# Optimization experiments

Measured on AMD Instinct MI355X. Metric: run time of the kernel, lower is better.

The kernel has to match this reference:

```python
import jax, jax.numpy as jnp
import numpy as np
import itertools

B, T, C, H = 2, 2048, 1024, 8
HD = C // H  # head_dim = 128


def _head_dirs():
    # 8 trigrams = vertices of cube {-1,+1}^3, L2-normalized (norm sqrt(3))
    signs = [-1.0, 1.0]
    tri = np.array(list(itertools.product(signs, repeat=3)), dtype=np.float32)
    tri = tri / np.linalg.norm(tri, axis=1, keepdims=True)
    return jnp.asarray(tri[:H])  # [H, 3]


def setup_inputs() -> dict:
    key = jax.random.key(0)
    ks = jax.random.split(key, 5)
    w = lambda k, sh: jax.random.normal(k, sh, dtype=jnp.float32) * 0.02
    return {
        "x": jax.random.normal(ks[0], (B, T, C), dtype=jnp.float32),
        "Wq": w(ks[1], (H * 3, C)),
        "Wk": w(ks[2], (H * 3, C)),
        "Wv": w(ks[3], (C, C)),
        "Wo": w(ks[4], (C, C)),
        "scale": jnp.asarray(1.0 / np.sqrt(3.0), dtype=jnp.float32),
    }


def reference(x, Wq, Wk, Wv, Wo, scale):
    Bb, Tt, Cc = x.shape
    dirs = _head_dirs()  # [H, 3] constant buffer
    # tiny 3-dim per-head Q/K projections
    q3 = (x @ Wq.T).reshape(Bb, Tt, H, 3).transpose(0, 2, 1, 3)  # [B,H,T,3]
    k3 = (x @ Wk.T).reshape(Bb, Tt, H, 3).transpose(0, 2, 1, 3)  # [B,H,T,3]
    v = (x @ Wv.T).reshape(Bb, Tt, H, HD).transpose(0, 2, 1, 3)  # [B,H,T,HD]
    # projections of q/k onto each head's trigram direction
    q_on_dir = jnp.einsum('bhtd,hd->bht', q3, dirs)  # [B,H,T]
    k_on_dir = jnp.einsum('bhtd,hd->bht', k3, dirs)  # [B,H,T]
    # scores = scaled 3-dim dot product + geometric outer-product bias
    scores = jnp.einsum('bhtd,bhsd->bhts', q3, k3) * scale \
        + q_on_dir[..., :, None] * k_on_dir[..., None, :]  # [B,H,T,T]
    causal = jnp.tril(jnp.ones((Tt, Tt), dtype=bool))
    scores = jnp.where(causal, scores, -jnp.inf)
    attn = jax.nn.softmax(scores, axis=-1)
    out = jnp.einsum('bhts,bhsd->bhtd', attn, v)  # [B,H,T,HD]
    out = out.transpose(0, 2, 1, 3).reshape(Bb, Tt, Cc)
    return out @ Wo.T
```

## Files before the change

### kernel.cpp

```cpp
#include <hip/hip_runtime.h>
#include <hip/hip_bf16.h>

#define B_  2
#define T_  2048
#define C_  1024
#define H_  8
#define HD_ 128
#define M_  (B_*T_)

typedef short  bf16x8 __attribute__((ext_vector_type(8)));
typedef float  f32x4  __attribute__((ext_vector_type(4)));
typedef unsigned short u16x8 __attribute__((ext_vector_type(8)));
typedef unsigned int   u32x4 __attribute__((ext_vector_type(4)));

typedef const __attribute__((address_space(1))) void* gas_ptr;
typedef __attribute__((address_space(3))) void*       las_ptr;

#define L2E_ 1.4426950408889634f

static __device__ __forceinline__ unsigned short f2bf(float f) {
    unsigned int u = __float_as_uint(f);
    u += 0x7fffu + ((u >> 16) & 1u);
    return (unsigned short)(u >> 16);
}
static __device__ __forceinline__ unsigned int rne_u32(float f) {
    unsigned int u = __float_as_uint(f);
    return u + 0x7fffu + ((u >> 16) & 1u);
}
static __device__ __forceinline__ float bf2f(unsigned short u) {
    return __uint_as_float(((unsigned int)u) << 16);
}
static __device__ __forceinline__ float exp2_fast(float x) {
#if __has_builtin(__builtin_amdgcn_exp2f)
    return __builtin_amdgcn_exp2f(x);
#else
    return exp2f(x);
#endif
}

__global__ __launch_bounds__(256) void k_convert_w(const float* __restrict__ Wv,
                                                   const float* __restrict__ Wo,
                                                   unsigned short* __restrict__ wvbf,
                                                   unsigned short* __restrict__ wobf) {
    int i = blockIdx.x * 256 + threadIdx.x;
    const float* src; unsigned short* dst; int off;
    if (i < 262144) { src = Wv; dst = wvbf; off = i; }
    else            { src = Wo; dst = wobf; off = i - 262144; }
    float4 v = reinterpret_cast<const float4*>(src)[off];
    ushort4 o;
    o.x = f2bf(v.x); o.y = f2bf(v.y); o.z = f2bf(v.z); o.w = f2bf(v.w);
    reinterpret_cast<ushort4*>(dst)[off] = o;
}

__global__ __launch_bounds__(256) void k_proj_qk(const float* __restrict__ x,
                                                 const float* __restrict__ Wq,
                                                 const float* __restrict__ Wk,
                                                 const float* __restrict__ scale_p,
                                                 float* __restrict__ qt,
                                                 float* __restrict__ kt,
                                                 unsigned short* __restrict__ xbf) {
    __shared__ __align__(16) float wl[48][260];
    __shared__ __align__(16) float xl[16][260];
    __shared__ float res[16][48];
    const int tid  = threadIdx.x;
    const int row0 = blockIdx.x << 4;
    const int r    = tid >> 4, sub = tid & 15;
    float a0 = 0.f, a1 = 0.f, a2 = 0.f;

    for (int ch = 0; ch < 4; ++ch) {
        const int k0 = ch * 256;
        #pragma unroll
        for (int i = 0; i < 12; ++i) {
            int fi = i * 256 + tid;
            int wr = fi >> 6, wc = (fi & 63) * 4;
            const float* src = (wr < 24) ? (Wq + (size_t)wr * C_) : (Wk + (size_t)(wr - 24) * C_);
            *reinterpret_cast<float4*>(&wl[wr][wc]) = *reinterpret_cast<const float4*>(src + k0 + wc);
        }
        #pragma unroll
        for (int i = 0; i < 4; ++i) {
            int fi = i * 256 + tid;
            int xr = fi >> 6, xc = (fi & 63) * 4;
            size_t goff = (size_t)(row0 + xr) * C_ + k0 + xc;
            float4 xv = *reinterpret_cast<const float4*>(x + goff);
            *reinterpret_cast<float4*>(&xl[xr][xc]) = xv;
            ushort4 o;
            o.x = f2bf(xv.x); o.y = f2bf(xv.y); o.z = f2bf(xv.z); o.w = f2bf(xv.w);
            *reinterpret_cast<ushort4*>(xbf + goff) = o;
        }
        __syncthreads();
        const int oc = sub * 3;
        #pragma unroll 4
        for (int k = 0; k < 256; k += 4) {
            float4 xv = *reinterpret_cast<const float4*>(&xl[r][k]);
            float4 w0 = *reinterpret_cast<const float4*>(&wl[oc + 0][k]);
            float4 w1 = *reinterpret_cast<const float4*>(&wl[oc + 1][k]);
            float4 w2 = *reinterpret_cast<const float4*>(&wl[oc + 2][k]);
            a0 += xv.x * w0.x + xv.y * w0.y + xv.z * w0.z + xv.w * w0.w;
            a1 += xv.x * w1.x + xv.y * w1.y + xv.z * w1.z + xv.w * w1.w;
            a2 += xv.x * w2.x + xv.y * w2.y + xv.z * w2.z + xv.w * w2.w;
        }
        __syncthreads();
    }
    res[r][sub * 3 + 0] = a0;
    res[r][sub * 3 + 1] = a1;
    res[r][sub * 3 + 2] = a2;
    __syncthreads();

    {
        const int rr = tid >> 4, s2 = tid & 15;
        const int isK = s2 >> 3, h = s2 & 7;
        const float r3 = 0.57735026918962576f;
        float d0 = (h & 4) ? r3 : -r3;
        float d1 = (h & 2) ? r3 : -r3;
        float d2 = (h & 1) ? r3 : -r3;
        const float* v3 = &res[rr][isK * 24 + h * 3];
        float a = v3[0], b = v3[1], c = v3[2];
        float ond = a * d0 + b * d1 + c * d2;
        float sc = scale_p[0];
        float4 ov = isK ? make_float4(a, b, c, ond)
                        : make_float4(a * sc * L2E_, b * sc * L2E_, c * sc * L2E_, ond * L2E_);
        float* dst = isK ? kt : qt;
        int grow = row0 + rr;
        int b_ = grow >> 11, t_idx = grow & (T_ - 1);
        reinterpret_cast<float4*>(dst)[(size_t)(b_ * H_ + h) * T_ + t_idx] = ov;
    }
}

template <int MODE>
__global__ __launch_bounds__(256) void k_gemm128x64(const unsigned short* __restrict__ A,
                                                    const unsigned short* __restrict__ Bw,
                                                    void* __restrict__ Cout,
                                                    int Mdim, int Ndim, int Kdim) {
    __shared__ __align__(16) unsigned short lds_a[8][128][8];
    __shared__ __align__(16) unsigned short lds_b[8][64][8];
    const int tid = threadIdx.x;
    const int nbn = Ndim >> 6;
    const int bm = (blockIdx.x / nbn) << 7;
    const int bn = (blockIdx.x % nbn) << 6;
    const int w = tid >> 6, l = tid & 63;
    const int wm = (w >> 1) << 6, wn = (w & 1) << 5;
    const int lh = l & 15, lq = l >> 4;

    f32x4 acc[4][2];
    #pragma unroll
    for (int i = 0; i < 4; ++i)
        #pragma unroll
        for (int j = 0; j < 2; ++j)
            acc[i][j] = (f32x4){0.f, 0.f, 0.f, 0.f};

    for (int k0 = 0; k0 < Kdim; k0 += 64) {
        #pragma unroll
        for (int p = 0; p < 4; ++p) {
            int flat = p * 256 + tid;
            int kq = flat >> 7, row = flat & 127;
            __builtin_amdgcn_global_load_lds((gas_ptr)(A + (size_t)(bm + row) * Kdim + k0 + kq * 8),
                (las_ptr)(&lds_a[0][0][0] + (size_t)flat * 8), 16, 0, 0);
        }
        #pragma unroll
        for (int p = 0; p < 2; ++p) {
            int flat = p * 256 + tid;
            int kq = flat >> 6, row = flat & 63;
            __builtin_amdgcn_global_load_lds((gas_ptr)(Bw + (size_t)(bn + row) * Kdim + k0 + kq * 8),
                (las_ptr)(&lds_b[0][0][0] + (size_t)flat * 8), 16, 0, 0);
        }
        __syncthreads();

        #pragma unroll
        for (int kk = 0; kk < 2; ++kk) {
            bf16x8 af[4], bfr[2];
            #pragma unroll
            for (int f = 0; f < 4; ++f)
                af[f] = *reinterpret_cast<const bf16x8*>(&lds_a[lq + 4 * kk][wm + f * 16 + lh][0]);
            #pragma unroll
            for (int f = 0; f < 2; ++f)
                bfr[f] = *reinterpret_cast<const bf16x8*>(&lds_b[lq + 4 * kk][wn + f * 16 + lh][0]);
            #pragma unroll
            for (int i = 0; i < 4; ++i)
                #pragma unroll
                for (int j = 0; j < 2; ++j)
                    acc[i][j] = __builtin_amdgcn_mfma_f32_16x16x32_bf16(af[i], bfr[j], acc[i][j], 0, 0, 0);
        }
        __syncthreads();
    }

    if constexpr (MODE == 0) {
        float* Cf = (float*)Cout;
        #pragma unroll
        for (int i = 0; i < 4; ++i) {
            int rbase = bm + wm + i * 16 + lq * 4;
            #pragma unroll
            for (int j = 0; j < 2; ++j) {
                int cidx = bn + wn + j * 16 + lh;
                #pragma unroll
                for (int r = 0; r < 4; ++r)
                    Cf[(size_t)(rbase + r) * Ndim + cidx] = acc[i][j][r];
            }
        }
    } else {
        __shared__ unsigned short ldsT[128][72];
        #pragma unroll
        for (int i = 0; i < 4; ++i)
            #pragma unroll
            for (int j = 0; j < 2; ++j)
                #pragma unroll
                for (int r = 0; r < 4; ++r)
                    ldsT[wm + i * 16 + lq * 4 + r][wn + j * 16 + lh] = f2bf(acc[i][j][r]);
        __syncthreads();
        unsigned short* vt_out = (unsigned short*)Cout;
        int c = tid & 63, part = tid >> 6;
        int b = bm >> 11, t0 = bm & (T_ - 1);
        unsigned short* dst = vt_out + ((size_t)b * C_ + bn + c) * T_ + t0 + part * 32;
        #pragma unroll
        for (int jj = 0; jj < 4; ++jj) {
            u16x8 v;
            #pragma unroll
            for (int k = 0; k < 8; ++k) v[k] = ldsT[part * 32 + jj * 8 + k][c];
            *reinterpret_cast<u16x8*>(dst + jj * 8) = v;
        }
    }
}

__global__ __launch_bounds__(256) void k_attn64(
        const float4* __restrict__ qt, const float4* __restrict__ kt,
        const unsigned short* __restrict__ vt,
        unsigned short* __restrict__ mpart,
        float2* __restrict__ mlbuf,
        int nsp, int lg2nsp) {
    __shared__ __align__(16) unsigned short lv[2][8192];
    __shared__ __align__(16) float4 lk[2][64];
    const int tid = threadIdx.x;
    const int w = tid >> 6, l = tid & 63;
    const int lh = l & 15, lg = l >> 4;
    const int bid = blockIdx.x;
    const int qb = 31 - (bid >> (4 + lg2nsp));
    const int sp = (bid >> 4) & (nsp - 1);
    const int bh = bid & 15;
    const int q0 = qb << 6;
    const int qrow = q0 + 4 * lh + w;
    const int nt = qb + 1;

    const float4* qtb = qt + (size_t)bh * T_;
    const float4* ktb = kt + (size_t)bh * T_;
    const unsigned short* vtb = vt + (size_t)bh * HD_ * T_;

    const unsigned short* vsrc[4];
    #pragma unroll
    for (int i = 0; i < 4; ++i) {
        int f = i * 256 + tid;
        vsrc[i] = vtb + (size_t)((((f >> 6) & 7) * 16) + (f & 15)) * T_
                      + ((f >> 9) << 5) + ((f >> 4) & 3) * 8;
    }

#define STAGE(ST, BUF) do {                                                    \
    int s0_ = (ST) << 6;                                                       \
    __builtin_amdgcn_global_load_lds((gas_ptr)(vsrc[0] + s0_),                 \
        (las_ptr)(&lv[BUF][0] + (size_t)(0 * 256 + tid) * 8), 16, 0, 0);       \
    __builtin_amdgcn_global_load_lds((gas_ptr)(vsrc[1] + s0_),                 \
        (las_ptr)(&lv[BUF][0] + (size_t)(1 * 256 + tid) * 8), 16, 0, 0);       \
    __builtin_amdgcn_global_load_lds((gas_ptr)(vsrc[2] + s0_),                 \
        (las_ptr)(&lv[BUF][0] + (size_t)(2 * 256 + tid) * 8), 16, 0, 0);       \
    __builtin_amdgcn_global_load_lds((gas_ptr)(vsrc[3] + s0_),                 \
        (las_ptr)(&lv[BUF][0] + (size_t)(3 * 256 + tid) * 8), 16, 0, 0);       \
    __builtin_amdgcn_global_load_lds((gas_ptr)(ktb + s0_ + l),                 \
        (las_ptr)(&lk[BUF][0]), 16, 0, 0);                                     \
} while (0)

    const float4 q4 = qtb[qrow];
    f32x4 acc[8];
    #pragma unroll
    for (int n = 0; n < 8; ++n) acc[n] = (f32x4){0.f, 0.f, 0.f, 0.f};
    float m = -1e30f, lsum = 0.f;

    if (sp < nt) STAGE(sp, 0);
    __syncthreads();

    int buf = 0;
    for (int st = sp; st < nt; st += nsp) {
        if (st + nsp < nt) STAGE(st + nsp, buf ^ 1);

        const int s0 = st << 6;
        const int c0 = s0 + lg * 8;
        const int c1 = s0 + 32 + lg * 8;

        float p[16];
        if (st != qb) {
            #pragma unroll
            for (int jj = 0; jj < 8; ++jj) {
                float4 k4 = lk[buf][lg * 8 + jj];
                p[jj] = fmaf(q4.x, k4.x, fmaf(q4.y, k4.y, fmaf(q4.z, k4.z, q4.w * k4.w)));
            }
            #pragma unroll
            for (int jj = 0; jj < 8; ++jj) {
                float4 k4 = lk[buf][32 + lg * 8 + jj];
                p[8 + jj] = fmaf(q4.x, k4.x, fmaf(q4.y, k4.y, fmaf(q4.z, k4.z, q4.w * k4.w)));
            }
        } else {
            #pragma unroll
            for (int jj = 0; jj < 8; ++jj) {
                float4 k4 = lk[buf][lg * 8 + jj];
                float sc = fmaf(q4.x, k4.x, fmaf(q4.y, k4.y, fmaf(q4.z, k4.z, q4.w * k4.w)));
                p[jj] = (c0 + jj > qrow) ? -1e30f : sc;
            }
            #pragma unroll
            for (int jj = 0; jj < 8; ++jj) {
                float4 k4 = lk[buf][32 + lg * 8 + jj];
                float sc = fmaf(q4.x, k4.x, fmaf(q4.y, k4.y, fmaf(q4.z, k4.z, q4.w * k4.w)));
                p[8 + jj] = (c1 + jj > qrow) ? -1e30f : sc;
            }
        }

        float ma = fmaxf(fmaxf(p[0], p[1]), p[2]);
        float mb = fmaxf(fmaxf(p[3], p[4]), p[5]);
        float mc = fmaxf(fmaxf(p[6], p[7]), p[8]);
        float md = fmaxf(fmaxf(p[9], p[10]), p[11]);
        float me = fmaxf(fmaxf(p[12], p[13]), p[14]);
        float mt = fmaxf(fmaxf(fmaxf(ma, mb), fmaxf(mc, md)), fmaxf(me, p[15]));
        mt = fmaxf(mt, __shfl_xor(mt, 16));
        mt = fmaxf(mt, __shfl_xor(mt, 32));
        if (__any(mt > m + 8.f)) {
            float mnew = fmaxf(m, mt);
            float corr = exp2_fast(m - mnew);
            m = mnew;
            lsum *= corr;
            float cc0 = __shfl(corr, 4 * lg + 0);
            float cc1 = __shfl(corr, 4 * lg + 1);
            float cc2 = __shfl(corr, 4 * lg + 2);
            float cc3 = __shfl(corr, 4 * lg + 3);
            #pragma unroll
            for (int n = 0; n < 8; ++n) {
                acc[n][0] *= cc0; acc[n][1] *= cc1; acc[n][2] *= cc2; acc[n][3] *= cc3;
            }
        }
        #pragma unroll
        for (int jj = 0; jj < 16; ++jj)
            p[jj] = exp2_fast(p[jj] - m);
        float sa = (p[0] + p[1] + p[2]) + (p[3] + p[4] + p[5]);
        float sb = (p[6] + p[7] + p[8]) + (p[9] + p[10] + p[11]);
        float ps = sa + sb + ((p[12] + p[13] + p[14]) + p[15]);
        ps += __shfl_xor(ps, 16);
        ps += __shfl_xor(ps, 32);
        lsum += ps;

        u32x4 w0, w1;
        #pragma unroll
        for (int i = 0; i < 4; ++i) {
            w0[i] = __builtin_amdgcn_perm(rne_u32(p[2 * i + 1]), rne_u32(p[2 * i]), 0x07060302u);
            w1[i] = __builtin_amdgcn_perm(rne_u32(p[8 + 2 * i + 1]), rne_u32(p[8 + 2 * i]), 0x07060302u);
        }
        bf16x8 pa0 = __builtin_bit_cast(bf16x8, w0);
        bf16x8 pa1 = __builtin_bit_cast(bf16x8, w1);

        #pragma unroll
        for (int n = 0; n < 8; ++n) {
            bf16x8 vf = *reinterpret_cast<const bf16x8*>(&lv[buf][(size_t)(n * 64 + lg * 16 + lh) * 8]);
            acc[n] = __builtin_amdgcn_mfma_f32_16x16x32_bf16(pa0, vf, acc[n], 0, 0, 0);
        }
        #pragma unroll
        for (int n = 0; n < 8; ++n) {
            bf16x8 vf = *reinterpret_cast<const bf16x8*>(&lv[buf][(size_t)(512 + n * 64 + lg * 16 + lh) * 8]);
            acc[n] = __builtin_amdgcn_mfma_f32_16x16x32_bf16(pa1, vf, acc[n], 0, 0, 0);
        }

        __syncthreads();
        buf ^= 1;
    }
#undef STAGE

    unsigned short* mp = mpart + (size_t)(sp * 16 + bh) * T_ * HD_;
    #pragma unroll
    for (int n = 0; n < 8; ++n) {
        #pragma unroll
        for (int r = 0; r < 4; ++r) {
            int row = q0 + 16 * lg + 4 * r + w;
            mp[(size_t)row * HD_ + n * 16 + lh] = f2bf(acc[n][r]);
        }
    }
    if (lg == 0)
        mlbuf[(size_t)(sp * 16 + bh) * T_ + qrow] = make_float2(m, lsum);
}

__global__ __launch_bounds__(256) void k_combine(const unsigned short* __restrict__ mpart,
                                                 const float2* __restrict__ mlbuf,
                                                 unsigned short* __restrict__ attnbf,
                                                 int nsp) {
    int idx = blockIdx.x * 256 + threadIdx.x;
    int bh = idx >> 16;
    int rem = idx & 65535;
    int t = rem >> 5, d0 = (rem & 31) * 4;
    float mg = -1e30f, den = 0.f;
    float ax = 0.f, ay = 0.f, az = 0.f, aw = 0.f;
    for (int s = 0; s < nsp; ++s) {
        float2 ml = mlbuf[(size_t)(s * 16 + bh) * T_ + t];
        ushort4 a = *reinterpret_cast<const ushort4*>(
            mpart + ((size_t)(s * 16 + bh) * T_ + t) * HD_ + d0);
        float mn = fmaxf(mg, ml.x);
        float cOld = exp2_fast(mg - mn);
        float cNew = exp2_fast(ml.x - mn);
        den = den * cOld + ml.y * cNew;
        ax = ax * cOld + bf2f(a.x) * cNew;
        ay = ay * cOld + bf2f(a.y) * cNew;
        az = az * cOld + bf2f(a.z) * cNew;
        aw = aw * cOld + bf2f(a.w) * cNew;
        mg = mn;
    }
    float inv = 1.f / den;
    int b = bh >> 3, h = bh & 7;
    ushort4 o;
    o.x = f2bf(ax * inv); o.y = f2bf(ay * inv);
    o.z = f2bf(az * inv); o.w = f2bf(aw * inv);
    *reinterpret_cast<ushort4*>(attnbf + ((size_t)(b * T_ + t) * C_ + h * HD_ + d0)) = o;
}

extern "C" void kernel_launch(void* const* d_in, const int* in_sizes, int n_in,
                              void* d_out, int out_size, void* d_ws, size_t ws_size,
                              hipStream_t stream) {
    const float* x     = (const float*)d_in[0];
    const float* Wq    = (const float*)d_in[1];
    const float* Wk    = (const float*)d_in[2];
    const float* Wv    = (const float*)d_in[3];
    const float* Wo    = (const float*)d_in[4];
    const float* scale = (const float*)d_in[5];
    float* out = (float*)d_out;

    const int nsp    = (ws_size >= 46137344) ? 4 : 2;
    const int lg2nsp = (nsp == 4) ? 2 : 1;

    char* ws = (char*)d_ws;
    size_t o = (size_t)nsp * 8388608;
    unsigned short* mpart  = (unsigned short*)(ws);
    unsigned short* xbf    = (unsigned short*)(ws);
    unsigned short* wvbf   = (unsigned short*)(ws + 8388608);
    float*          qt     = (float*)(ws + o);
    float*          kt     = (float*)(ws + o + 524288);
    unsigned short* vt     = (unsigned short*)(ws + o + 1048576);
    unsigned short* attnbf = (unsigned short*)(ws + o + 1048576);
    unsigned short* wobf   = (unsigned short*)(ws + o + 9437184);
    float2*         mlbuf  = (float2*)(ws + o + 11534336);

    k_convert_w<<<2048, 256, 0, stream>>>(Wv, Wo, wvbf, wobf);

    k_proj_qk<<<M_ / 16, 256, 0, stream>>>(x, Wq, Wk, scale, qt, kt, xbf);

    k_gemm128x64<2><<<(M_ / 128) * (C_ / 64), 256, 0, stream>>>(xbf, wvbf, (void*)vt, M_, C_, C_);

    k_attn64<<<32 * nsp * 16, 256, 0, stream>>>(
        reinterpret_cast<const float4*>(qt), reinterpret_cast<const float4*>(kt), vt,
        mpart, mlbuf, nsp, lg2nsp);

    k_combine<<<4096, 256, 0, stream>>>(mpart, mlbuf, attnbf, nsp);

    k_gemm128x64<0><<<(M_ / 128) * (C_ / 64), 256, 0, stream>>>(attnbf, wobf, (void*)out, M_, C_, C_);
}
```

Before: 133.8 us.

## Double-buffer LDS tiles in the 128x64 GEMM to overlap loads with MFMA

Adds a second LDS buffer for the A and B tiles of the bf16 GEMM kernel. The next K-slice is issued with global_load_lds while MFMAs run on the current buffer, with one barrier per iteration instead of two. The goal is to hide global memory latency in the projection GEMMs. In exchange, the kernel's LDS use roughly doubles, which can lower how many blocks fit per CU.

```diff
diff --git a/kernel.cpp b/kernel.cpp
--- a/kernel.cpp
+++ b/kernel.cpp
@@ -131,8 +131,8 @@
                                                     const unsigned short* __restrict__ Bw,
                                                     void* __restrict__ Cout,
                                                     int Mdim, int Ndim, int Kdim) {
-    __shared__ __align__(16) unsigned short lds_a[8][128][8];
-    __shared__ __align__(16) unsigned short lds_b[8][64][8];
+    __shared__ __align__(16) unsigned short lds_a[2][8][128][8];
+    __shared__ __align__(16) unsigned short lds_b[2][8][64][8];
     const int tid = threadIdx.x;
     const int nbn = Ndim >> 6;
     const int bm = (blockIdx.x / nbn) << 7;
@@ -141,6 +141,25 @@
     const int wm = (w >> 1) << 6, wn = (w & 1) << 5;
     const int lh = l & 15, lq = l >> 4;
 
+#define GSTAGE(K0, BUF) do {                                                          \
+    _Pragma("unroll")                                                                 \
+    for (int p_ = 0; p_ < 4; ++p_) {                                                  \
+        int flat_ = p_ * 256 + tid;                                                   \
+        int kq_ = flat_ >> 7, row_ = flat_ & 127;                                     \
+        __builtin_amdgcn_global_load_lds(                                             \
+            (gas_ptr)(A + (size_t)(bm + row_) * Kdim + (K0) + kq_ * 8),               \
+            (las_ptr)(&lds_a[BUF][0][0][0] + (size_t)flat_ * 8), 16, 0, 0);           \
+    }                                                                                 \
+    _Pragma("unroll")                                                                 \
+    for (int p_ = 0; p_ < 2; ++p_) {                                                  \
+        int flat_ = p_ * 256 + tid;                                                   \
+        int kq_ = flat_ >> 6, row_ = flat_ & 63;                                      \
+        __builtin_amdgcn_global_load_lds(                                             \
+            (gas_ptr)(Bw + (size_t)(bn + row_) * Kdim + (K0) + kq_ * 8),              \
+            (las_ptr)(&lds_b[BUF][0][0][0] + (size_t)flat_ * 8), 16, 0, 0);           \
+    }                                                                                 \
+} while (0)
+
     f32x4 acc[4][2];
     #pragma unroll
     for (int i = 0; i < 4; ++i)
@@ -148,32 +167,22 @@
         for (int j = 0; j < 2; ++j)
             acc[i][j] = (f32x4){0.f, 0.f, 0.f, 0.f};
 
+    GSTAGE(0, 0);
+    __syncthreads();
+
+    int buf = 0;
     for (int k0 = 0; k0 < Kdim; k0 += 64) {
-        #pragma unroll
-        for (int p = 0; p < 4; ++p) {
-            int flat = p * 256 + tid;
-            int kq = flat >> 7, row = flat & 127;
-            __builtin_amdgcn_global_load_lds((gas_ptr)(A + (size_t)(bm + row) * Kdim + k0 + kq * 8),
-                (las_ptr)(&lds_a[0][0][0] + (size_t)flat * 8), 16, 0, 0);
-        }
-        #pragma unroll
-        for (int p = 0; p < 2; ++p) {
-            int flat = p * 256 + tid;
-            int kq = flat >> 6, row = flat & 63;
-            __builtin_amdgcn_global_load_lds((gas_ptr)(Bw + (size_t)(bn + row) * Kdim + k0 + kq * 8),
-                (las_ptr)(&lds_b[0][0][0] + (size_t)flat * 8), 16, 0, 0);
-        }
-        __syncthreads();
+        if (k0 + 64 < Kdim) GSTAGE(k0 + 64, buf ^ 1);
 
         #pragma unroll
         for (int kk = 0; kk < 2; ++kk) {
             bf16x8 af[4], bfr[2];
             #pragma unroll
             for (int f = 0; f < 4; ++f)
-                af[f] = *reinterpret_cast<const bf16x8*>(&lds_a[lq + 4 * kk][wm + f * 16 + lh][0]);
+                af[f] = *reinterpret_cast<const bf16x8*>(&lds_a[buf][lq + 4 * kk][wm + f * 16 + lh][0]);
             #pragma unroll
             for (int f = 0; f < 2; ++f)
-                bfr[f] = *reinterpret_cast<const bf16x8*>(&lds_b[lq + 4 * kk][wn + f * 16 + lh][0]);
+                bfr[f] = *reinterpret_cast<const bf16x8*>(&lds_b[buf][lq + 4 * kk][wn + f * 16 + lh][0]);
             #pragma unroll
             for (int i = 0; i < 4; ++i)
                 #pragma unroll
@@ -181,7 +190,9 @@
                     acc[i][j] = __builtin_amdgcn_mfma_f32_16x16x32_bf16(af[i], bfr[j], acc[i][j], 0, 0, 0);
         }
         __syncthreads();
-    }
+        buf ^= 1;
+    }
+#undef GSTAGE
 
     if constexpr (MODE == 0) {
         float* Cf = (float*)Cout;
```

After: 134.9 us. No clear change (+0.8%).
